# Optimization experiments

Hardware: AMD Instinct MI355X
Metric: run time of the kernel (lower is better)

Reference implementation:

```python
import jax, jax.numpy as jnp
import numpy as np

# Keras ConvLSTM2D defaults: activation=tanh, recurrent_activation=hard_sigmoid,
# gate order i, f, c, o; padding='same'; BatchNormalization: axis=-1, eps=1e-3.

def hard_sigmoid(x):
    return jnp.clip(0.2 * x + 0.5, 0.0, 1.0)

def conv2d(x, w):
    # x: (N, H, W, Cin), w: (kh, kw, Cin, Cout), stride 1, SAME padding
    return jax.lax.conv_general_dilated(
        x, w, window_strides=(1, 1), padding='SAME',
        dimension_numbers=('NHWC', 'HWIO', 'NHWC'))

def conv_lstm(x_seq, Wx, Wh, b):
    # x_seq: (B, T, H, W, Cin); Wx: (k,k,Cin,4F); Wh: (k,k,F,4F); b: (4F,)
    B, T, H, W, Cin = x_seq.shape
    F = Wh.shape[2]
    # Input-to-gate convs are time-independent: do all T steps as one batched conv.
    xg = conv2d(x_seq.reshape(B * T, H, W, Cin), Wx).reshape(B, T, H, W, 4 * F) + b
    xg = jnp.moveaxis(xg, 1, 0)  # (T, B, H, W, 4F)
    h0 = jnp.zeros((B, H, W, F), x_seq.dtype)

    def step(carry, g_in):
        h, c = carry
        g = g_in + conv2d(h, Wh)  # (B, H, W, 4F)
        i, f, cc, o = jnp.split(g, 4, axis=-1)
        i = hard_sigmoid(i)
        f = hard_sigmoid(f)
        o = hard_sigmoid(o)
        c = f * c + i * jnp.tanh(cc)
        h = o * jnp.tanh(c)
        return (h, c), h

    (h, c), ys = jax.lax.scan(step, (h0, h0), xg)
    return jnp.moveaxis(ys, 0, 1), h, c  # (B,T,H,W,F), (B,H,W,F), (B,H,W,F)

def batchnorm_train(x, gamma, beta, eps=1e-3):
    # training=True: batch statistics over all axes but channels (biased var)
    mean = jnp.mean(x, axis=(0, 1, 2, 3), keepdims=True)
    var = jnp.var(x, axis=(0, 1, 2, 3), keepdims=True)
    return gamma * (x - mean) * jax.lax.rsqrt(var + eps) + beta

def setup_inputs() -> dict:
    key = jax.random.key(0)
    ks = jax.random.split(key, 9)
    B, T, H, W, Cin, F, k = 8, 10, 48, 48, 16, 64, 3
    s = 0.05
    return {
        'x':      jax.random.normal(ks[0], (B, T, H, W, Cin), jnp.float32),
        'Wx1':    jax.random.normal(ks[1], (k, k, Cin, 4 * F), jnp.float32) * s,
        'Wh1':    jax.random.normal(ks[2], (k, k, F, 4 * F), jnp.float32) * s,
        'b1':     jnp.zeros((4 * F,), jnp.float32),
        'gamma1': jnp.ones((F,), jnp.float32),
        'beta1':  jnp.zeros((F,), jnp.float32),
        'Wx2':    jax.random.normal(ks[3], (k, k, F, 4 * F), jnp.float32) * s,
        'Wh2':    jax.random.normal(ks[4], (k, k, F, 4 * F), jnp.float32) * s,
        'b2':     jnp.zeros((4 * F,), jnp.float32),
    }

def reference(x, Wx1, Wh1, b1, gamma1, beta1, Wx2, Wh2, b2):
    seq1, h1, c1 = conv_lstm(x, Wx1, Wh1, b1)
    seq1 = batchnorm_train(seq1, gamma1, beta1)
    _, h2, c2 = conv_lstm(seq1, Wx2, Wh2, b2)
    # states = [[h1, c1], [h2, c2]] flattened
    return (h1, c1, h2, c2)
```

## Files before the change

### kernel.cpp

```cpp
#include <hip/hip_runtime.h>
#include <hip/hip_bf16.h>

typedef short bf16x8 __attribute__((ext_vector_type(8)));
typedef float f32x4  __attribute__((ext_vector_type(4)));

constexpr int B = 8, T = 10, F = 64, CO = 256;
constexpr long IMGPIX      = 48 * 48;
constexpr long STATE_ELEMS = (long)B * IMGPIX * F;
constexpr long SEQ_ELEMS   = (long)T * STATE_ELEMS;
constexpr float BN_INVN    = 1.0f / (float)(B * T * IMGPIX);

__device__ __forceinline__ float  b2f(ushort u) { return __uint_as_float(((unsigned)u) << 16); }
__device__ __forceinline__ ushort f2b(float f) {
    unsigned x = __float_as_uint(f);
    return (ushort)((x + 0x7fffu + ((x >> 16) & 1u)) >> 16);
}
__device__ __forceinline__ float hsig(float x) { return fminf(fmaxf(0.2f * x + 0.5f, 0.f), 1.f); }
__device__ __forceinline__ float tanh_f(float v) {
    return 1.f - 2.f / (__expf(2.f * v) + 1.f);
}

union V16 { uint4 u; bf16x8 b; };

template<int CIN_A, int CPAD, bool FIRST, bool STATS, bool BNIN, bool OUT>
__global__ __launch_bounds__(256, 3) void convlstm_step(
    const ushort* __restrict__ inA, long strideA,
    const ushort* __restrict__ inB,
    const ushort* __restrict__ Wsw,
    const float*  __restrict__ bias,
    float*  __restrict__ cState,
    ushort* __restrict__ hOut,
    ushort* __restrict__ seqOut,
    float*  __restrict__ stats,
    const float* __restrict__ gamma,
    const float* __restrict__ beta,
    float*  __restrict__ outF)
{
    constexpr int CIN_TOT = CIN_A + 64;
    constexpr int K   = 9 * CIN_TOT;
    constexpr int KS  = (K + 31) / 32;
    constexpr int KSH = (KS + 1) / 2;
    constexpr int KP  = KS * 32;
    constexpr int PATCHB = 3 * 50 * CPAD * 2;
    constexpr int SMEMB  = PATCHB > 26368 ? PATCHB : 26368;
    __shared__ __align__(16) unsigned char smem[SMEMB];
    __shared__ float bnsc[64], bnsh[64];

    const int bid  = blockIdx.x;
    const int img  = bid / 96;
    const int rem  = bid % 96;
    const int y    = rem >> 1;
    const int half = rem & 1;
    const int tid = threadIdx.x, wid = tid >> 6, l = tid & 63;
    const int lm = l & 15, lk8 = (l >> 4) * 8;

    if constexpr (BNIN) {
        if (tid < 64) {
            const float mean = stats[tid] * BN_INVN;
            const float var  = stats[64 + tid] * BN_INVN - mean * mean;
            const float sc   = gamma[tid] * rsqrtf(var + 1e-3f);
            bnsc[tid] = sc;
            bnsh[tid] = beta[tid] - mean * sc;
        }
        __syncthreads();
    }

    const ushort* aBase = inA + (size_t)img * strideA;
    const ushort* bBase = inB + (size_t)img * IMGPIX * 64;
    constexpr int CA8 = CIN_A / 8;
    for (int e = tid; e < 3 * 48 * CA8; e += 256) {
        const int r = e / (48 * CA8), qq = e % (48 * CA8);
        const int col = qq / CA8, ci0 = (qq % CA8) * 8;
        const int gy = y + r - 1;
        uint4 v = make_uint4(0, 0, 0, 0);
        if (gy >= 0 && gy < 48) {
            v = *(const uint4*)(aBase + ((size_t)gy * 48 + col) * CIN_A + ci0);
            if constexpr (BNIN) {
                ushort* u = (ushort*)&v;
#pragma unroll
                for (int j = 0; j < 8; ++j)
                    u[j] = f2b(b2f(u[j]) * bnsc[ci0 + j] + bnsh[ci0 + j]);
            }
        }
        *(uint4*)(smem + ((r * 50 + col + 1) * CPAD + ci0) * 2) = v;
    }
    for (int e = tid; e < 3 * 48 * 8; e += 256) {
        const int r = e / (48 * 8), qq = e % (48 * 8);
        const int col = qq / 8, ci0 = (qq % 8) * 8;
        uint4 v = make_uint4(0, 0, 0, 0);
        if constexpr (!FIRST) {
            const int gy = y + r - 1;
            if (gy >= 0 && gy < 48)
                v = *(const uint4*)(bBase + ((size_t)gy * 48 + col) * 64 + ci0);
        }
        *(uint4*)(smem + ((r * 50 + col + 1) * CPAD + CIN_A + ci0) * 2) = v;
    }
    constexpr int CT8 = CIN_TOT / 8;
    for (int e = tid; e < 3 * 2 * CT8; e += 256) {
        const int r = e / (2 * CT8), qq = e % (2 * CT8);
        const int dc = (qq / CT8) ? 49 : 0, ci0 = (qq % CT8) * 8;
        *(uint4*)(smem + ((r * 50 + dc) * CPAD + ci0) * 2) = make_uint4(0, 0, 0, 0);
    }
    __syncthreads();

    const int q      = 2 * half + (wid & 1);
    const int kshard = wid >> 1;

    f32x4 acc[3][4] = {};

#pragma unroll
    for (int ksl = 0; ksl < KSH; ++ksl) {
        const int ks = 2 * ksl + kshard;
        if (ks < KS) {
            V16 bf[4];
#pragma unroll
            for (int nr = 0; nr < 4; ++nr) {
                const int ntile = nr * 4 + q;
                bf[nr].u = *(const uint4*)(Wsw + ((size_t)((ntile * KS + ks) * 64) + l) * 8);
            }
            V16 af[3];
#pragma unroll
            for (int m = 0; m < 3; ++m) {
                const int k   = ks * 32 + lk8;
                const int tap = k / CIN_TOT, ci0 = k % CIN_TOT;
                const int ky  = tap / 3, kx = tap - 3 * (tap / 3);
                const int c   = m * 16 + lm + kx;
                uint4 v = *(const uint4*)(smem + ((ky * 50 + c) * CPAD + ci0) * 2);
                if (KP > K && ks == KS - 1 && k >= K) v = make_uint4(0, 0, 0, 0);
                af[m].u = v;
            }
#pragma unroll
            for (int m = 0; m < 3; ++m)
#pragma unroll
                for (int nr = 0; nr < 4; ++nr)
                    acc[m][nr] = __builtin_amdgcn_mfma_f32_16x16x32_bf16(
                        af[m].b, bf[nr].b, acc[m][nr], 0, 0, 0);
        }
    }

    __syncthreads();
    float* gbuf = (float*)smem;
    float* sred = (float*)(smem + 25344);
    const int fl = (q & 1) * 16 + lm;

    if (kshard == 0) {
#pragma unroll
        for (int nr = 0; nr < 4; ++nr) {
            const float bv = bias[nr * 64 + q * 16 + lm];
#pragma unroll
            for (int m = 0; m < 3; ++m)
#pragma unroll
                for (int r = 0; r < 4; ++r) {
                    const int pixel = m * 16 + (l >> 4) * 4 + r;
                    gbuf[pixel * 132 + nr * 32 + fl] = acc[m][nr][r] + bv;
                }
        }
    }
    __syncthreads();
    if (kshard == 1) {
#pragma unroll
        for (int nr = 0; nr < 4; ++nr)
#pragma unroll
            for (int m = 0; m < 3; ++m)
#pragma unroll
                for (int r = 0; r < 4; ++r) {
                    const int pixel = m * 16 + (l >> 4) * 4 + r;
                    gbuf[pixel * 132 + nr * 32 + fl] += acc[m][nr][r];
                }
    }
    __syncthreads();

    float s1 = 0.f, s2 = 0.f;
    const size_t rowBase = (size_t)img * IMGPIX + (size_t)y * 48;
#pragma unroll
    for (int it = 0; it < 6; ++it) {
        const int idx = it * 256 + tid;
        const int p = idx >> 5, fr = idx & 31;
        const float gi = gbuf[p * 132 + fr];
        const float gf = gbuf[p * 132 + 32 + fr];
        const float gc = gbuf[p * 132 + 64 + fr];
        const float go = gbuf[p * 132 + 96 + fr];
        const size_t off = (rowBase + p) * 64 + half * 32 + fr;
        const float cold = FIRST ? 0.f : cState[off];
        const float cn = hsig(gf) * cold + hsig(gi) * tanh_f(gc);
        const float hn = hsig(go) * tanh_f(cn);
        cState[off] = cn;
        hOut[off]   = f2b(hn);
        if constexpr (STATS) { seqOut[off] = f2b(hn); s1 += hn; s2 += hn * hn; }
        if constexpr (OUT)   { outF[off] = hn; outF[STATE_ELEMS + off] = cn; }
    }

    if constexpr (STATS) {
        s1 += __shfl_xor(s1, 32);
        s2 += __shfl_xor(s2, 32);
        if (l < 32) { sred[wid * 64 + l] = s1; sred[wid * 64 + 32 + l] = s2; }
        __syncthreads();
        if (tid < 64) {
            const int kind = tid >> 5, fr = tid & 31;
            const float v = sred[kind * 32 + fr] + sred[64 + kind * 32 + fr]
                          + sred[128 + kind * 32 + fr] + sred[192 + kind * 32 + fr];
            atomicAdd(&stats[kind * 64 + half * 32 + fr], v);
        }
    }
}

__device__ __forceinline__ ushort swz_elem(
    const float* __restrict__ Wx, const float* __restrict__ Wh,
    int CIN_A, int KS, int idx)
{
    const int K = 9 * (CIN_A + 64);
    const int j = idx & 7, lw = (idx >> 3) & 63, rest = idx >> 9;
    const int ks = rest % KS, ntile = rest / KS;
    const int n = ntile * 16 + (lw & 15);
    const int k = ks * 32 + ((lw >> 4) & 3) * 8 + j;
    if (k >= K) return (ushort)0;
    const int CT = CIN_A + 64;
    const int tap = k / CT, ci = k % CT;
    const float v = (ci < CIN_A) ? Wx[((size_t)tap * CIN_A + ci) * CO + n]
                                 : Wh[((size_t)tap * 64 + (ci - CIN_A)) * CO + n];
    return f2b(v);
}

__global__ __launch_bounds__(256) void prep_kernel(
    const float* __restrict__ x,
    const float* __restrict__ Wx1, const float* __restrict__ Wh1,
    const float* __restrict__ Wx2, const float* __restrict__ Wh2,
    ushort* __restrict__ xb, ushort* __restrict__ wc1, ushort* __restrict__ wc2,
    float* __restrict__ stats)
{
    constexpr int N0 = 368640;
    constexpr int N1 = 16 * 23 * 512;
    constexpr int N2 = 16 * 36 * 512;
    const int gid = blockIdx.x * 256 + threadIdx.x;
    if (gid < N0) {
        const float4 a = ((const float4*)x)[(size_t)gid * 2];
        const float4 b = ((const float4*)x)[(size_t)gid * 2 + 1];
        ushort o[8] = { f2b(a.x), f2b(a.y), f2b(a.z), f2b(a.w),
                        f2b(b.x), f2b(b.y), f2b(b.z), f2b(b.w) };
        *(uint4*)(xb + (size_t)gid * 8) = *(const uint4*)o;
    } else if (gid < N0 + N1) {
        wc1[gid - N0] = swz_elem(Wx1, Wh1, 16, 23, gid - N0);
    } else if (gid < N0 + N1 + N2) {
        wc2[gid - N0 - N1] = swz_elem(Wx2, Wh2, 64, 36, gid - N0 - N1);
    } else if (gid < N0 + N1 + N2 + 128) {
        stats[gid - N0 - N1 - N2] = 0.f;
    }
}

extern "C" void kernel_launch(void* const* d_in, const int* in_sizes, int n_in,
                              void* d_out, int out_size, void* d_ws, size_t ws_size,
                              hipStream_t stream)
{
    const float* x      = (const float*)d_in[0];
    const float* Wx1    = (const float*)d_in[1];
    const float* Wh1    = (const float*)d_in[2];
    const float* b1     = (const float*)d_in[3];
    const float* gamma1 = (const float*)d_in[4];
    const float* beta1  = (const float*)d_in[5];
    const float* Wx2    = (const float*)d_in[6];
    const float* Wh2    = (const float*)d_in[7];
    const float* b2     = (const float*)d_in[8];

    unsigned char* w = (unsigned char*)d_ws;
    ushort* seq1 = (ushort*)w;  w += 23592960;
    ushort* xb   = (ushort*)w;  w += 5898240;
    ushort* wc1  = (ushort*)w;  w += 376832;
    ushort* wc2  = (ushort*)w;  w += 589824;
    ushort* hb1a = (ushort*)w;  w += 2359296;
    ushort* hb1b = (ushort*)w;  w += 2359296;
    ushort* hb2a = (ushort*)w;  w += 2359296;
    ushort* hb2b = (ushort*)w;  w += 2359296;
    float*  c1   = (float*)w;   w += 4718592;
    float*  c2   = (float*)w;   w += 4718592;
    float*  stats = (float*)w;  w += 512;

    prep_kernel<<<3329, 256, 0, stream>>>(x, Wx1, Wh1, Wx2, Wh2, xb, wc1, wc2, stats);

    const long xStride = (long)T * IMGPIX * 16;
    ushort* hp1[2] = { hb1a, hb1b };

    convlstm_step<16, 88, true, true, false, false><<<768, 256, 0, stream>>>(
        xb, xStride, hp1[0], wc1, b1, c1, hp1[1],
        seq1, stats, nullptr, nullptr, nullptr);
    for (int t = 1; t < 9; ++t)
        convlstm_step<16, 88, false, true, false, false><<<768, 256, 0, stream>>>(
            xb + (size_t)t * IMGPIX * 16, xStride, hp1[t & 1], wc1, b1, c1, hp1[(t + 1) & 1],
            seq1 + (size_t)t * STATE_ELEMS, stats, nullptr, nullptr, nullptr);
    convlstm_step<16, 88, false, true, false, true><<<768, 256, 0, stream>>>(
        xb + (size_t)9 * IMGPIX * 16, xStride, hp1[1], wc1, b1, c1, hp1[0],
        seq1 + (size_t)9 * STATE_ELEMS, stats, nullptr, nullptr, (float*)d_out);

    ushort* hp2[2] = { hb2a, hb2b };
    convlstm_step<64, 136, true, false, true, false><<<768, 256, 0, stream>>>(
        seq1, IMGPIX * 64, hp2[0], wc2, b2, c2, hp2[1],
        nullptr, stats, gamma1, beta1, nullptr);
    for (int t = 1; t < 9; ++t)
        convlstm_step<64, 136, false, false, true, false><<<768, 256, 0, stream>>>(
            seq1 + (size_t)t * STATE_ELEMS, IMGPIX * 64, hp2[t & 1], wc2, b2, c2, hp2[(t + 1) & 1],
            nullptr, stats, gamma1, beta1, nullptr);
    convlstm_step<64, 136, false, false, true, true><<<768, 256, 0, stream>>>(
        seq1 + (size_t)9 * STATE_ELEMS, IMGPIX * 64, hp2[1], wc2, b2, c2, hp2[0],
        nullptr, stats, gamma1, beta1, (float*)d_out + 2 * STATE_ELEMS);
}
```

Measured before the change: 413.9 us.

## Retile ConvLSTM step to two rows by one gate-quarter per block with LDS swizzle

Each block now computes two output rows for one 16-channel quarter of every gate, instead of one row with a K-split across waves. This removes the cross-wave accumulator reduction pass and its extra barrier, and each weight fragment is reused across six pixel tiles instead of three. Layer 2 uses an unpadded 128-channel LDS row with an XOR swizzle to avoid bank conflicts in place of padding. In exchange the input patch grows to four rows, each block reloads the halo for its own channel quarter, and the occupancy hint of 3 blocks per CU is dropped.

```diff
diff --git a/kernel.cpp b/kernel.cpp
--- a/kernel.cpp
+++ b/kernel.cpp
@@ -7,7 +7,6 @@
 constexpr int B = 8, T = 10, F = 64, CO = 256;
 constexpr long IMGPIX      = 48 * 48;
 constexpr long STATE_ELEMS = (long)B * IMGPIX * F;
-constexpr long SEQ_ELEMS   = (long)T * STATE_ELEMS;
 constexpr float BN_INVN    = 1.0f / (float)(B * T * IMGPIX);
 
 __device__ __forceinline__ float  b2f(ushort u) { return __uint_as_float(((unsigned)u) << 16); }
@@ -22,8 +21,8 @@
 
 union V16 { uint4 u; bf16x8 b; };
 
-template<int CIN_A, int CPAD, bool FIRST, bool STATS, bool BNIN, bool OUT>
-__global__ __launch_bounds__(256, 3) void convlstm_step(
+template<int CIN_A, int CPAD, bool SWZ, bool FIRST, bool STATS, bool BNIN, bool OUT>
+__global__ __launch_bounds__(256) void convlstm_step(
     const ushort* __restrict__ inA, long strideA,
     const ushort* __restrict__ inB,
     const ushort* __restrict__ Wsw,
@@ -39,18 +38,19 @@
     constexpr int CIN_TOT = CIN_A + 64;
     constexpr int K   = 9 * CIN_TOT;
     constexpr int KS  = (K + 31) / 32;
-    constexpr int KSH = (KS + 1) / 2;
     constexpr int KP  = KS * 32;
-    constexpr int PATCHB = 3 * 50 * CPAD * 2;
-    constexpr int SMEMB  = PATCHB > 26368 ? PATCHB : 26368;
+    constexpr int PATCHB = 4 * 50 * CPAD * 2;
+    constexpr int GBUFB  = 96 * 68 * 4;
+    constexpr int SMEMB  = PATCHB > GBUFB ? PATCHB : GBUFB;
     __shared__ __align__(16) unsigned char smem[SMEMB];
+    __shared__ float sred[4][2][16];
     __shared__ float bnsc[64], bnsh[64];
 
-    const int bid  = blockIdx.x;
-    const int img  = bid / 96;
-    const int rem  = bid % 96;
-    const int y    = rem >> 1;
-    const int half = rem & 1;
+    const int bid = blockIdx.x;
+    const int img = bid / 96;
+    const int rem = bid % 96;
+    const int y2  = rem >> 2;
+    const int q   = rem & 3;
     const int tid = threadIdx.x, wid = tid >> 6, l = tid & 63;
     const int lm = l & 15, lk8 = (l >> 4) * 8;
 
@@ -65,13 +65,19 @@
         __syncthreads();
     }
 
+    auto lds_off = [&](int r, int dc, int ci0) -> int {
+        int byte = ((r * 50 + dc) * CPAD + ci0) * 2;
+        if constexpr (SWZ) byte ^= (dc & 7) << 4;
+        return byte;
+    };
+
     const ushort* aBase = inA + (size_t)img * strideA;
     const ushort* bBase = inB + (size_t)img * IMGPIX * 64;
     constexpr int CA8 = CIN_A / 8;
-    for (int e = tid; e < 3 * 48 * CA8; e += 256) {
+    for (int e = tid; e < 4 * 48 * CA8; e += 256) {
         const int r = e / (48 * CA8), qq = e % (48 * CA8);
         const int col = qq / CA8, ci0 = (qq % CA8) * 8;
-        const int gy = y + r - 1;
+        const int gy = y2 * 2 + r - 1;
         uint4 v = make_uint4(0, 0, 0, 0);
         if (gy >= 0 && gy < 48) {
             v = *(const uint4*)(aBase + ((size_t)gy * 48 + col) * CIN_A + ci0);
@@ -82,105 +88,75 @@
                     u[j] = f2b(b2f(u[j]) * bnsc[ci0 + j] + bnsh[ci0 + j]);
             }
         }
-        *(uint4*)(smem + ((r * 50 + col + 1) * CPAD + ci0) * 2) = v;
-    }
-    for (int e = tid; e < 3 * 48 * 8; e += 256) {
+        *(uint4*)(smem + lds_off(r, col + 1, ci0)) = v;
+    }
+    for (int e = tid; e < 4 * 48 * 8; e += 256) {
         const int r = e / (48 * 8), qq = e % (48 * 8);
         const int col = qq / 8, ci0 = (qq % 8) * 8;
         uint4 v = make_uint4(0, 0, 0, 0);
         if constexpr (!FIRST) {
-            const int gy = y + r - 1;
+            const int gy = y2 * 2 + r - 1;
             if (gy >= 0 && gy < 48)
                 v = *(const uint4*)(bBase + ((size_t)gy * 48 + col) * 64 + ci0);
         }
-        *(uint4*)(smem + ((r * 50 + col + 1) * CPAD + CIN_A + ci0) * 2) = v;
+        *(uint4*)(smem + lds_off(r, col + 1, CIN_A + ci0)) = v;
     }
     constexpr int CT8 = CIN_TOT / 8;
-    for (int e = tid; e < 3 * 2 * CT8; e += 256) {
+    for (int e = tid; e < 4 * 2 * CT8; e += 256) {
         const int r = e / (2 * CT8), qq = e % (2 * CT8);
         const int dc = (qq / CT8) ? 49 : 0, ci0 = (qq % CT8) * 8;
-        *(uint4*)(smem + ((r * 50 + dc) * CPAD + ci0) * 2) = make_uint4(0, 0, 0, 0);
+        *(uint4*)(smem + lds_off(r, dc, ci0)) = make_uint4(0, 0, 0, 0);
     }
     __syncthreads();
 
-    const int q      = 2 * half + (wid & 1);
-    const int kshard = wid >> 1;
-
-    f32x4 acc[3][4] = {};
-
-#pragma unroll
-    for (int ksl = 0; ksl < KSH; ++ksl) {
-        const int ks = 2 * ksl + kshard;
-        if (ks < KS) {
-            V16 bf[4];
-#pragma unroll
-            for (int nr = 0; nr < 4; ++nr) {
-                const int ntile = nr * 4 + q;
-                bf[nr].u = *(const uint4*)(Wsw + ((size_t)((ntile * KS + ks) * 64) + l) * 8);
-            }
-            V16 af[3];
-#pragma unroll
-            for (int m = 0; m < 3; ++m) {
-                const int k   = ks * 32 + lk8;
-                const int tap = k / CIN_TOT, ci0 = k % CIN_TOT;
-                const int ky  = tap / 3, kx = tap - 3 * (tap / 3);
-                const int c   = m * 16 + lm + kx;
-                uint4 v = *(const uint4*)(smem + ((ky * 50 + c) * CPAD + ci0) * 2);
-                if (KP > K && ks == KS - 1 && k >= K) v = make_uint4(0, 0, 0, 0);
-                af[m].u = v;
-            }
-#pragma unroll
-            for (int m = 0; m < 3; ++m)
-#pragma unroll
-                for (int nr = 0; nr < 4; ++nr)
-                    acc[m][nr] = __builtin_amdgcn_mfma_f32_16x16x32_bf16(
-                        af[m].b, bf[nr].b, acc[m][nr], 0, 0, 0);
-        }
+    const int ntile = wid * 4 + q;
+    f32x4 acc[6] = {};
+
+#pragma unroll
+    for (int ks = 0; ks < KS; ++ks) {
+        V16 bf;
+        bf.u = *(const uint4*)(Wsw + ((size_t)(ntile * KS + ks) * 64 + l) * 8);
+        const int k   = ks * 32 + lk8;
+        const int tap = k / CIN_TOT, ci0 = k % CIN_TOT;
+        const int ky  = tap / 3, kx = tap - 3 * (tap / 3);
+        V16 af[6];
+#pragma unroll
+        for (int m = 0; m < 6; ++m) {
+            const int sr = (m < 3) ? 0 : 1;
+            const int fm = (m < 3) ? m : m - 3;
+            const int dcc = fm * 16 + lm + kx;
+            uint4 v = *(const uint4*)(smem + lds_off(sr + ky, dcc, ci0));
+            if (KP > K && ks == KS - 1 && k >= K) v = make_uint4(0, 0, 0, 0);
+            af[m].u = v;
+        }
+#pragma unroll
+        for (int m = 0; m < 6; ++m)
+            acc[m] = __builtin_amdgcn_mfma_f32_16x16x32_bf16(af[m].b, bf.b, acc[m], 0, 0, 0);
     }
 
     __syncthreads();
     float* gbuf = (float*)smem;
-    float* sred = (float*)(smem + 25344);
-    const int fl = (q & 1) * 16 + lm;
-
-    if (kshard == 0) {
-#pragma unroll
-        for (int nr = 0; nr < 4; ++nr) {
-            const float bv = bias[nr * 64 + q * 16 + lm];
-#pragma unroll
-            for (int m = 0; m < 3; ++m)
-#pragma unroll
-                for (int r = 0; r < 4; ++r) {
-                    const int pixel = m * 16 + (l >> 4) * 4 + r;
-                    gbuf[pixel * 132 + nr * 32 + fl] = acc[m][nr][r] + bv;
-                }
-        }
-    }
+    const float bv = bias[wid * 64 + q * 16 + lm];
+#pragma unroll
+    for (int m = 0; m < 6; ++m)
+#pragma unroll
+        for (int r = 0; r < 4; ++r) {
+            const int pixel = m * 16 + (l >> 4) * 4 + r;
+            gbuf[pixel * 68 + wid * 16 + lm] = acc[m][r] + bv;
+        }
     __syncthreads();
-    if (kshard == 1) {
-#pragma unroll
-        for (int nr = 0; nr < 4; ++nr)
-#pragma unroll
-            for (int m = 0; m < 3; ++m)
-#pragma unroll
-                for (int r = 0; r < 4; ++r) {
-                    const int pixel = m * 16 + (l >> 4) * 4 + r;
-                    gbuf[pixel * 132 + nr * 32 + fl] += acc[m][nr][r];
-                }
-    }
-    __syncthreads();
 
     float s1 = 0.f, s2 = 0.f;
-    const size_t rowBase = (size_t)img * IMGPIX + (size_t)y * 48;
+    const size_t rowBase = (size_t)img * IMGPIX + (size_t)y2 * 96;
 #pragma unroll
     for (int it = 0; it < 6; ++it) {
         const int idx = it * 256 + tid;
-        const int p = idx >> 5, fr = idx & 31;
-        const float gi = gbuf[p * 132 + fr];
-        const float gf = gbuf[p * 132 + 32 + fr];
-        const float gc = gbuf[p * 132 + 64 + fr];
-        const float go = gbuf[p * 132 + 96 + fr];
-        const size_t off = (rowBase + p) * 64 + half * 32 + fr;
+        const int p = idx >> 4, fr = idx & 15;
+        const float gi = gbuf[p * 68 + fr];
+        const float gf = gbuf[p * 68 + 16 + fr];
+        const float gc = gbuf[p * 68 + 32 + fr];
+        const float go = gbuf[p * 68 + 48 + fr];
+        const size_t off = (rowBase + p) * 64 + q * 16 + fr;
         const float cold = FIRST ? 0.f : cState[off];
         const float cn = hsig(gf) * cold + hsig(gi) * tanh_f(gc);
         const float hn = hsig(go) * tanh_f(cn);
@@ -191,15 +167,15 @@
     }
 
     if constexpr (STATS) {
-        s1 += __shfl_xor(s1, 32);
-        s2 += __shfl_xor(s2, 32);
-        if (l < 32) { sred[wid * 64 + l] = s1; sred[wid * 64 + 32 + l] = s2; }
+        s1 += __shfl_xor(s1, 16);  s2 += __shfl_xor(s2, 16);
+        s1 += __shfl_xor(s1, 32);  s2 += __shfl_xor(s2, 32);
+        if (l < 16) { sred[wid][0][l] = s1; sred[wid][1][l] = s2; }
         __syncthreads();
-        if (tid < 64) {
-            const int kind = tid >> 5, fr = tid & 31;
-            const float v = sred[kind * 32 + fr] + sred[64 + kind * 32 + fr]
-                          + sred[128 + kind * 32 + fr] + sred[192 + kind * 32 + fr];
-            atomicAdd(&stats[kind * 64 + half * 32 + fr], v);
+        if (tid < 32) {
+            const int kind = tid >> 4, fr = tid & 15;
+            const float v = sred[0][kind][fr] + sred[1][kind][fr]
+                          + sred[2][kind][fr] + sred[3][kind][fr];
+            atomicAdd(&stats[kind * 64 + q * 16 + fr], v);
         }
     }
 }
@@ -279,26 +255,26 @@
     const long xStride = (long)T * IMGPIX * 16;
     ushort* hp1[2] = { hb1a, hb1b };
 
-    convlstm_step<16, 88, true, true, false, false><<<768, 256, 0, stream>>>(
+    convlstm_step<16, 88, false, true, true, false, false><<<768, 256, 0, stream>>>(
         xb, xStride, hp1[0], wc1, b1, c1, hp1[1],
         seq1, stats, nullptr, nullptr, nullptr);
     for (int t = 1; t < 9; ++t)
-        convlstm_step<16, 88, false, true, false, false><<<768, 256, 0, stream>>>(
+        convlstm_step<16, 88, false, false, true, false, false><<<768, 256, 0, stream>>>(
             xb + (size_t)t * IMGPIX * 16, xStride, hp1[t & 1], wc1, b1, c1, hp1[(t + 1) & 1],
             seq1 + (size_t)t * STATE_ELEMS, stats, nullptr, nullptr, nullptr);
-    convlstm_step<16, 88, false, true, false, true><<<768, 256, 0, stream>>>(
+    convlstm_step<16, 88, false, false, true, false, true><<<768, 256, 0, stream>>>(
         xb + (size_t)9 * IMGPIX * 16, xStride, hp1[1], wc1, b1, c1, hp1[0],
         seq1 + (size_t)9 * STATE_ELEMS, stats, nullptr, nullptr, (float*)d_out);
 
     ushort* hp2[2] = { hb2a, hb2b };
-    convlstm_step<64, 136, true, false, true, false><<<768, 256, 0, stream>>>(
+    convlstm_step<64, 128, true, true, false, true, false><<<768, 256, 0, stream>>>(
         seq1, IMGPIX * 64, hp2[0], wc2, b2, c2, hp2[1],
         nullptr, stats, gamma1, beta1, nullptr);
     for (int t = 1; t < 9; ++t)
-        convlstm_step<64, 136, false, false, true, false><<<768, 256, 0, stream>>>(
+        convlstm_step<64, 128, true, false, false, true, false><<<768, 256, 0, stream>>>(
             seq1 + (size_t)t * STATE_ELEMS, IMGPIX * 64, hp2[t & 1], wc2, b2, c2, hp2[(t + 1) & 1],
             nullptr, stats, gamma1, beta1, nullptr);
-    convlstm_step<64, 136, false, false, true, true><<<768, 256, 0, stream>>>(
+    convlstm_step<64, 128, true, false, false, true, true><<<768, 256, 0, stream>>>(
         seq1 + (size_t)9 * STATE_ELEMS, IMGPIX * 64, hp2[1], wc2, b2, c2, hp2[0],
         nullptr, stats, gamma1, beta1, (float*)d_out + 2 * STATE_ELEMS);
 }
```

New measurement: 465.1 us. 12.4% more time.

## Hoist input-to-gate convolutions out of recurrence into batched precompute kernel

Applied to the files above, without the earlier changes.

Splits each ConvLSTM step into a one-shot batched input convolution over all timesteps, writing fp32 gate preactivations plus bias to a workspace buffer. The per-step recurrent kernel then only convolves the hidden state and adds the precomputed gates. This shrinks the serial per-step MFMA work and makes the input conv fully parallel across time. The cost is a large fp32 intermediate buffer, which adds write and read traffic.

```diff
diff --git a/kernel.cpp b/kernel.cpp
--- a/kernel.cpp
+++ b/kernel.cpp
@@ -7,7 +7,7 @@
 constexpr int B = 8, T = 10, F = 64, CO = 256;
 constexpr long IMGPIX      = 48 * 48;
 constexpr long STATE_ELEMS = (long)B * IMGPIX * F;
-constexpr long SEQ_ELEMS   = (long)T * STATE_ELEMS;
+constexpr long GX_IMG      = IMGPIX * 256;
 constexpr float BN_INVN    = 1.0f / (float)(B * T * IMGPIX);
 
 __device__ __forceinline__ float  b2f(ushort u) { return __uint_as_float(((unsigned)u) << 16); }
@@ -22,33 +22,30 @@
 
 union V16 { uint4 u; bf16x8 b; };
 
-template<int CIN_A, int CPAD, bool FIRST, bool STATS, bool BNIN, bool OUT>
-__global__ __launch_bounds__(256, 3) void convlstm_step(
-    const ushort* __restrict__ inA, long strideA,
-    const ushort* __restrict__ inB,
+template<int CIN, int CPAD, bool BNIN>
+__global__ __launch_bounds__(256, 3) void conv_gates(
+    const ushort* __restrict__ in,
     const ushort* __restrict__ Wsw,
     const float*  __restrict__ bias,
-    float*  __restrict__ cState,
-    ushort* __restrict__ hOut,
-    ushort* __restrict__ seqOut,
-    float*  __restrict__ stats,
+    float* __restrict__ gx,
+    int permute,
+    const float* __restrict__ stats,
     const float* __restrict__ gamma,
-    const float* __restrict__ beta,
-    float*  __restrict__ outF)
+    const float* __restrict__ beta)
 {
-    constexpr int CIN_TOT = CIN_A + 64;
-    constexpr int K   = 9 * CIN_TOT;
+    constexpr int K   = 9 * CIN;
     constexpr int KS  = (K + 31) / 32;
     constexpr int KSH = (KS + 1) / 2;
     constexpr int KP  = KS * 32;
     constexpr int PATCHB = 3 * 50 * CPAD * 2;
-    constexpr int SMEMB  = PATCHB > 26368 ? PATCHB : 26368;
+    constexpr int GBUFB  = 48 * 132 * 4;
+    constexpr int SMEMB  = PATCHB > GBUFB ? PATCHB : GBUFB;
     __shared__ __align__(16) unsigned char smem[SMEMB];
     __shared__ float bnsc[64], bnsh[64];
 
-    const int bid  = blockIdx.x;
-    const int img  = bid / 96;
-    const int rem  = bid % 96;
+    const int bid = blockIdx.x;
+    const int img_in = bid / 96;
+    const int rem = bid % 96;
     const int y    = rem >> 1;
     const int half = rem & 1;
     const int tid = threadIdx.x, wid = tid >> 6, l = tid & 63;
@@ -65,16 +62,15 @@
         __syncthreads();
     }
 
-    const ushort* aBase = inA + (size_t)img * strideA;
-    const ushort* bBase = inB + (size_t)img * IMGPIX * 64;
-    constexpr int CA8 = CIN_A / 8;
-    for (int e = tid; e < 3 * 48 * CA8; e += 256) {
-        const int r = e / (48 * CA8), qq = e % (48 * CA8);
-        const int col = qq / CA8, ci0 = (qq % CA8) * 8;
+    const ushort* aBase = in + (size_t)img_in * IMGPIX * CIN;
+    constexpr int C8 = CIN / 8;
+    for (int e = tid; e < 3 * 48 * C8; e += 256) {
+        const int r = e / (48 * C8), qq = e % (48 * C8);
+        const int col = qq / C8, ci0 = (qq % C8) * 8;
         const int gy = y + r - 1;
         uint4 v = make_uint4(0, 0, 0, 0);
         if (gy >= 0 && gy < 48) {
-            v = *(const uint4*)(aBase + ((size_t)gy * 48 + col) * CIN_A + ci0);
+            v = *(const uint4*)(aBase + ((size_t)gy * 48 + col) * CIN + ci0);
             if constexpr (BNIN) {
                 ushort* u = (ushort*)&v;
 #pragma unroll
@@ -84,6 +80,111 @@
         }
         *(uint4*)(smem + ((r * 50 + col + 1) * CPAD + ci0) * 2) = v;
     }
+    for (int e = tid; e < 3 * 2 * C8; e += 256) {
+        const int r = e / (2 * C8), qq = e % (2 * C8);
+        const int dc = (qq / C8) ? 49 : 0, ci0 = (qq % C8) * 8;
+        *(uint4*)(smem + ((r * 50 + dc) * CPAD + ci0) * 2) = make_uint4(0, 0, 0, 0);
+    }
+    __syncthreads();
+
+    const int q      = 2 * half + (wid & 1);
+    const int kshard = wid >> 1;
+    f32x4 acc[3][4] = {};
+
+#pragma unroll
+    for (int ksl = 0; ksl < KSH; ++ksl) {
+        const int ks = 2 * ksl + kshard;
+        if (ks < KS) {
+            V16 bf[4];
+#pragma unroll
+            for (int nr = 0; nr < 4; ++nr) {
+                const int ntile = nr * 4 + q;
+                bf[nr].u = *(const uint4*)(Wsw + ((size_t)((ntile * KS + ks) * 64) + l) * 8);
+            }
+            V16 af[3];
+#pragma unroll
+            for (int m = 0; m < 3; ++m) {
+                const int k   = ks * 32 + lk8;
+                const int tap = k / CIN, ci0 = k % CIN;
+                const int ky  = tap / 3, kx = tap - 3 * (tap / 3);
+                const int c   = m * 16 + lm + kx;
+                uint4 v = *(const uint4*)(smem + ((ky * 50 + c) * CPAD + ci0) * 2);
+                if (KP > K && ks == KS - 1 && k >= K) v = make_uint4(0, 0, 0, 0);
+                af[m].u = v;
+            }
+#pragma unroll
+            for (int m = 0; m < 3; ++m)
+#pragma unroll
+                for (int nr = 0; nr < 4; ++nr)
+                    acc[m][nr] = __builtin_amdgcn_mfma_f32_16x16x32_bf16(
+                        af[m].b, bf[nr].b, acc[m][nr], 0, 0, 0);
+        }
+    }
+
+    __syncthreads();
+    float* gbuf = (float*)smem;
+    const int fl = (q & 1) * 16 + lm;
+    if (kshard == 0) {
+#pragma unroll
+        for (int nr = 0; nr < 4; ++nr)
+#pragma unroll
+            for (int m = 0; m < 3; ++m)
+#pragma unroll
+                for (int r = 0; r < 4; ++r) {
+                    const int pixel = m * 16 + (l >> 4) * 4 + r;
+                    gbuf[pixel * 132 + nr * 32 + fl] = acc[m][nr][r];
+                }
+    }
+    __syncthreads();
+    if (kshard == 1) {
+#pragma unroll
+        for (int nr = 0; nr < 4; ++nr)
+#pragma unroll
+            for (int m = 0; m < 3; ++m)
+#pragma unroll
+                for (int r = 0; r < 4; ++r) {
+                    const int pixel = m * 16 + (l >> 4) * 4 + r;
+                    gbuf[pixel * 132 + nr * 32 + fl] += acc[m][nr][r];
+                }
+    }
+    __syncthreads();
+
+    const long slab = permute ? (long)(img_in % 10) * 8 + img_in / 10 : (long)img_in;
+    float* gxp = gx + slab * GX_IMG + (long)y * 48 * 256;
+#pragma unroll
+    for (int it = 0; it < 24; ++it) {
+        const int idx = it * 256 + tid;
+        const int p = idx >> 7, c = idx & 127;
+        const int nr = c >> 5, flc = c & 31;
+        const int ch = nr * 64 + half * 32 + flc;
+        gxp[p * 256 + ch] = gbuf[p * 132 + c] + bias[ch];
+    }
+}
+
+template<bool FIRST, bool STATS, bool OUT>
+__global__ __launch_bounds__(256, 3) void rec_step(
+    const float*  __restrict__ gx,
+    const ushort* __restrict__ hIn,
+    const ushort* __restrict__ Wsw,
+    float*  __restrict__ cState,
+    ushort* __restrict__ hOut,
+    ushort* __restrict__ seqOut,
+    float*  __restrict__ stats,
+    float*  __restrict__ outF)
+{
+    constexpr int CIN = 64, CPAD = 72, KS = 18, KSH = 9;
+    constexpr int SMEMB = 26368;
+    __shared__ __align__(16) unsigned char smem[SMEMB];
+
+    const int bid = blockIdx.x;
+    const int img = bid / 96;
+    const int rem = bid % 96;
+    const int y    = rem >> 1;
+    const int half = rem & 1;
+    const int tid = threadIdx.x, wid = tid >> 6, l = tid & 63;
+    const int lm = l & 15, lk8 = (l >> 4) * 8;
+
+    const ushort* bBase = hIn + (size_t)img * IMGPIX * 64;
     for (int e = tid; e < 3 * 48 * 8; e += 256) {
         const int r = e / (48 * 8), qq = e % (48 * 8);
         const int col = qq / 8, ci0 = (qq % 8) * 8;
@@ -93,68 +194,59 @@
             if (gy >= 0 && gy < 48)
                 v = *(const uint4*)(bBase + ((size_t)gy * 48 + col) * 64 + ci0);
         }
-        *(uint4*)(smem + ((r * 50 + col + 1) * CPAD + CIN_A + ci0) * 2) = v;
-    }
-    constexpr int CT8 = CIN_TOT / 8;
-    for (int e = tid; e < 3 * 2 * CT8; e += 256) {
-        const int r = e / (2 * CT8), qq = e % (2 * CT8);
-        const int dc = (qq / CT8) ? 49 : 0, ci0 = (qq % CT8) * 8;
+        *(uint4*)(smem + ((r * 50 + col + 1) * CPAD + ci0) * 2) = v;
+    }
+    for (int e = tid; e < 3 * 2 * 8; e += 256) {
+        const int r = e / 16, qq = e % 16;
+        const int dc = (qq / 8) ? 49 : 0, ci0 = (qq % 8) * 8;
         *(uint4*)(smem + ((r * 50 + dc) * CPAD + ci0) * 2) = make_uint4(0, 0, 0, 0);
     }
     __syncthreads();
 
     const int q      = 2 * half + (wid & 1);
     const int kshard = wid >> 1;
-
     f32x4 acc[3][4] = {};
 
 #pragma unroll
     for (int ksl = 0; ksl < KSH; ++ksl) {
         const int ks = 2 * ksl + kshard;
-        if (ks < KS) {
-            V16 bf[4];
-#pragma unroll
-            for (int nr = 0; nr < 4; ++nr) {
-                const int ntile = nr * 4 + q;
-                bf[nr].u = *(const uint4*)(Wsw + ((size_t)((ntile * KS + ks) * 64) + l) * 8);
-            }
-            V16 af[3];
-#pragma unroll
-            for (int m = 0; m < 3; ++m) {
-                const int k   = ks * 32 + lk8;
-                const int tap = k / CIN_TOT, ci0 = k % CIN_TOT;
-                const int ky  = tap / 3, kx = tap - 3 * (tap / 3);
-                const int c   = m * 16 + lm + kx;
-                uint4 v = *(const uint4*)(smem + ((ky * 50 + c) * CPAD + ci0) * 2);
-                if (KP > K && ks == KS - 1 && k >= K) v = make_uint4(0, 0, 0, 0);
-                af[m].u = v;
-            }
-#pragma unroll
-            for (int m = 0; m < 3; ++m)
-#pragma unroll
-                for (int nr = 0; nr < 4; ++nr)
-                    acc[m][nr] = __builtin_amdgcn_mfma_f32_16x16x32_bf16(
-                        af[m].b, bf[nr].b, acc[m][nr], 0, 0, 0);
-        }
+        V16 bf[4];
+#pragma unroll
+        for (int nr = 0; nr < 4; ++nr) {
+            const int ntile = nr * 4 + q;
+            bf[nr].u = *(const uint4*)(Wsw + ((size_t)((ntile * KS + ks) * 64) + l) * 8);
+        }
+        V16 af[3];
+#pragma unroll
+        for (int m = 0; m < 3; ++m) {
+            const int k   = ks * 32 + lk8;
+            const int tap = k / CIN, ci0 = k % CIN;
+            const int ky  = tap / 3, kx = tap - 3 * (tap / 3);
+            const int c   = m * 16 + lm + kx;
+            af[m].u = *(const uint4*)(smem + ((ky * 50 + c) * CPAD + ci0) * 2);
+        }
+#pragma unroll
+        for (int m = 0; m < 3; ++m)
+#pragma unroll
+            for (int nr = 0; nr < 4; ++nr)
+                acc[m][nr] = __builtin_amdgcn_mfma_f32_16x16x32_bf16(
+                    af[m].b, bf[nr].b, acc[m][nr], 0, 0, 0);
     }
 
     __syncthreads();
     float* gbuf = (float*)smem;
     float* sred = (float*)(smem + 25344);
     const int fl = (q & 1) * 16 + lm;
-
     if (kshard == 0) {
 #pragma unroll
-        for (int nr = 0; nr < 4; ++nr) {
-            const float bv = bias[nr * 64 + q * 16 + lm];
+        for (int nr = 0; nr < 4; ++nr)
 #pragma unroll
             for (int m = 0; m < 3; ++m)
 #pragma unroll
                 for (int r = 0; r < 4; ++r) {
                     const int pixel = m * 16 + (l >> 4) * 4 + r;
-                    gbuf[pixel * 132 + nr * 32 + fl] = acc[m][nr][r] + bv;
+                    gbuf[pixel * 132 + nr * 32 + fl] = acc[m][nr][r];
                 }
-        }
     }
     __syncthreads();
     if (kshard == 1) {
@@ -172,15 +264,17 @@
 
     float s1 = 0.f, s2 = 0.f;
     const size_t rowBase = (size_t)img * IMGPIX + (size_t)y * 48;
+    const float* gxrow = gx + ((size_t)img * IMGPIX + (size_t)y * 48) * 256;
 #pragma unroll
     for (int it = 0; it < 6; ++it) {
         const int idx = it * 256 + tid;
         const int p = idx >> 5, fr = idx & 31;
-        const float gi = gbuf[p * 132 + fr];
-        const float gf = gbuf[p * 132 + 32 + fr];
-        const float gc = gbuf[p * 132 + 64 + fr];
-        const float go = gbuf[p * 132 + 96 + fr];
-        const size_t off = (rowBase + p) * 64 + half * 32 + fr;
+        const int chb = half * 32 + fr;
+        const float gi = gbuf[p * 132 +       fr] + gxrow[p * 256 +       chb];
+        const float gf = gbuf[p * 132 +  32 + fr] + gxrow[p * 256 +  64 + chb];
+        const float gc = gbuf[p * 132 +  64 + fr] + gxrow[p * 256 + 128 + chb];
+        const float go = gbuf[p * 132 +  96 + fr] + gxrow[p * 256 + 192 + chb];
+        const size_t off = (rowBase + p) * 64 + chb;
         const float cold = FIRST ? 0.f : cState[off];
         const float cn = hsig(gf) * cold + hsig(gi) * tanh_f(gc);
         const float hn = hsig(go) * tanh_f(cn);
@@ -204,33 +298,31 @@
     }
 }
 
-__device__ __forceinline__ ushort swz_elem(
-    const float* __restrict__ Wx, const float* __restrict__ Wh,
-    int CIN_A, int KS, int idx)
+__device__ __forceinline__ ushort swz_w(
+    const float* __restrict__ W, int CIN, int KS, int idx)
 {
-    const int K = 9 * (CIN_A + 64);
+    const int K = 9 * CIN;
     const int j = idx & 7, lw = (idx >> 3) & 63, rest = idx >> 9;
     const int ks = rest % KS, ntile = rest / KS;
     const int n = ntile * 16 + (lw & 15);
     const int k = ks * 32 + ((lw >> 4) & 3) * 8 + j;
     if (k >= K) return (ushort)0;
-    const int CT = CIN_A + 64;
-    const int tap = k / CT, ci = k % CT;
-    const float v = (ci < CIN_A) ? Wx[((size_t)tap * CIN_A + ci) * CO + n]
-                                 : Wh[((size_t)tap * 64 + (ci - CIN_A)) * CO + n];
-    return f2b(v);
+    const int tap = k / CIN, ci = k % CIN;
+    return f2b(W[((size_t)tap * CIN + ci) * CO + n]);
 }
 
 __global__ __launch_bounds__(256) void prep_kernel(
     const float* __restrict__ x,
     const float* __restrict__ Wx1, const float* __restrict__ Wh1,
     const float* __restrict__ Wx2, const float* __restrict__ Wh2,
-    ushort* __restrict__ xb, ushort* __restrict__ wc1, ushort* __restrict__ wc2,
+    ushort* __restrict__ xb,
+    ushort* __restrict__ wx1, ushort* __restrict__ wh1,
+    ushort* __restrict__ wx2, ushort* __restrict__ wh2,
     float* __restrict__ stats)
 {
     constexpr int N0 = 368640;
-    constexpr int N1 = 16 * 23 * 512;
-    constexpr int N2 = 16 * 36 * 512;
+    constexpr int N1 = 16 * 5 * 512;
+    constexpr int N2 = 16 * 18 * 512;
     const int gid = blockIdx.x * 256 + threadIdx.x;
     if (gid < N0) {
         const float4 a = ((const float4*)x)[(size_t)gid * 2];
@@ -239,11 +331,15 @@
                         f2b(b.x), f2b(b.y), f2b(b.z), f2b(b.w) };
         *(uint4*)(xb + (size_t)gid * 8) = *(const uint4*)o;
     } else if (gid < N0 + N1) {
-        wc1[gid - N0] = swz_elem(Wx1, Wh1, 16, 23, gid - N0);
+        wx1[gid - N0] = swz_w(Wx1, 16, 5, gid - N0);
     } else if (gid < N0 + N1 + N2) {
-        wc2[gid - N0 - N1] = swz_elem(Wx2, Wh2, 64, 36, gid - N0 - N1);
-    } else if (gid < N0 + N1 + N2 + 128) {
-        stats[gid - N0 - N1 - N2] = 0.f;
+        wh1[gid - N0 - N1] = swz_w(Wh1, 64, 18, gid - N0 - N1);
+    } else if (gid < N0 + N1 + 2 * N2) {
+        wx2[gid - N0 - N1 - N2] = swz_w(Wx2, 64, 18, gid - N0 - N1 - N2);
+    } else if (gid < N0 + N1 + 3 * N2) {
+        wh2[gid - N0 - N1 - 2 * N2] = swz_w(Wh2, 64, 18, gid - N0 - N1 - 2 * N2);
+    } else if (gid < N0 + N1 + 3 * N2 + 128) {
+        stats[gid - N0 - N1 - 3 * N2] = 0.f;
     }
 }
 
@@ -262,10 +358,13 @@
     const float* b2     = (const float*)d_in[8];
 
     unsigned char* w = (unsigned char*)d_ws;
+    float*  gx   = (float*)w;   w += 188743680;
     ushort* seq1 = (ushort*)w;  w += 23592960;
     ushort* xb   = (ushort*)w;  w += 5898240;
-    ushort* wc1  = (ushort*)w;  w += 376832;
-    ushort* wc2  = (ushort*)w;  w += 589824;
+    ushort* wx1  = (ushort*)w;  w += 81920;
+    ushort* wh1  = (ushort*)w;  w += 294912;
+    ushort* wx2  = (ushort*)w;  w += 294912;
+    ushort* wh2  = (ushort*)w;  w += 294912;
     ushort* hb1a = (ushort*)w;  w += 2359296;
     ushort* hb1b = (ushort*)w;  w += 2359296;
     ushort* hb2a = (ushort*)w;  w += 2359296;
@@ -274,31 +373,34 @@
     float*  c2   = (float*)w;   w += 4718592;
     float*  stats = (float*)w;  w += 512;
 
-    prep_kernel<<<3329, 256, 0, stream>>>(x, Wx1, Wh1, Wx2, Wh2, xb, wc1, wc2, stats);
-
-    const long xStride = (long)T * IMGPIX * 16;
+    prep_kernel<<<3329, 256, 0, stream>>>(x, Wx1, Wh1, Wx2, Wh2,
+                                          xb, wx1, wh1, wx2, wh2, stats);
+
+    conv_gates<16, 24, false><<<7680, 256, 0, stream>>>(
+        xb, wx1, b1, gx, 1, nullptr, nullptr, nullptr);
+
     ushort* hp1[2] = { hb1a, hb1b };
-
-    convlstm_step<16, 88, true, true, false, false><<<768, 256, 0, stream>>>(
-        xb, xStride, hp1[0], wc1, b1, c1, hp1[1],
-        seq1, stats, nullptr, nullptr, nullptr);
+    rec_step<true, true, false><<<768, 256, 0, stream>>>(
+        gx, hp1[0], wh1, c1, hp1[1], seq1, stats, nullptr);
     for (int t = 1; t < 9; ++t)
-        convlstm_step<16, 88, false, true, false, false><<<768, 256, 0, stream>>>(
-            xb + (size_t)t * IMGPIX * 16, xStride, hp1[t & 1], wc1, b1, c1, hp1[(t + 1) & 1],
-            seq1 + (size_t)t * STATE_ELEMS, stats, nullptr, nullptr, nullptr);
-    convlstm_step<16, 88, false, true, false, true><<<768, 256, 0, stream>>>(
-        xb + (size_t)9 * IMGPIX * 16, xStride, hp1[1], wc1, b1, c1, hp1[0],
-        seq1 + (size_t)9 * STATE_ELEMS, stats, nullptr, nullptr, (float*)d_out);
+        rec_step<false, true, false><<<768, 256, 0, stream>>>(
+            gx + (size_t)t * 8 * GX_IMG, hp1[t & 1], wh1, c1, hp1[(t + 1) & 1],
+            seq1 + (size_t)t * STATE_ELEMS, stats, nullptr);
+    rec_step<false, true, true><<<768, 256, 0, stream>>>(
+        gx + (size_t)9 * 8 * GX_IMG, hp1[1], wh1, c1, hp1[0],
+        seq1 + (size_t)9 * STATE_ELEMS, stats, (float*)d_out);
+
+    conv_gates<64, 72, true><<<7680, 256, 0, stream>>>(
+        seq1, wx2, b2, gx, 0, stats, gamma1, beta1);
 
     ushort* hp2[2] = { hb2a, hb2b };
-    convlstm_step<64, 136, true, false, true, false><<<768, 256, 0, stream>>>(
-        seq1, IMGPIX * 64, hp2[0], wc2, b2, c2, hp2[1],
-        nullptr, stats, gamma1, beta1, nullptr);
+    rec_step<true, false, false><<<768, 256, 0, stream>>>(
+        gx, hp2[0], wh2, c2, hp2[1], nullptr, stats, nullptr);
     for (int t = 1; t < 9; ++t)
-        convlstm_step<64, 136, false, false, true, false><<<768, 256, 0, stream>>>(
-            seq1 + (size_t)t * STATE_ELEMS, IMGPIX * 64, hp2[t & 1], wc2, b2, c2, hp2[(t + 1) & 1],
-            nullptr, stats, gamma1, beta1, nullptr);
-    convlstm_step<64, 136, false, false, true, true><<<768, 256, 0, stream>>>(
-        seq1 + (size_t)9 * STATE_ELEMS, IMGPIX * 64, hp2[1], wc2, b2, c2, hp2[0],
-        nullptr, stats, gamma1, beta1, (float*)d_out + 2 * STATE_ELEMS);
-}
+        rec_step<false, false, false><<<768, 256, 0, stream>>>(
+            gx + (size_t)t * 8 * GX_IMG, hp2[t & 1], wh2, c2, hp2[(t + 1) & 1],
+            nullptr, stats, nullptr);
+    rec_step<false, false, true><<<768, 256, 0, stream>>>(
+        gx + (size_t)9 * 8 * GX_IMG, hp2[1], wh2, c2, hp2[0],
+        nullptr, stats, (float*)d_out + 2 * STATE_ELEMS);
+}
```

New measurement: 475.4 us. +14.9%, slower.
